# Optimization experiments

Hardware: AMD Instinct MI355X
Metric: run time of the kernel (lower is better)

## Reference

```python
import jax, jax.numpy as jnp
import numpy as np
from jax import lax

B, T = 4, 1024
V, C, H, L = 50257, 768, 12, 12
D = C // H           # head size = 64
FF = 4 * C           # ffn hidden = 3072
EPS = 1e-5


def setup_inputs() -> dict:
    key = jax.random.key(0)
    ks = jax.random.split(key, 20)
    s = 0.02
    inp = {
        'x': jax.random.randint(ks[0], (B, T), 0, V, dtype=jnp.int32),
        'y': jax.random.randint(ks[1], (B, T), 0, V, dtype=jnp.int32),
        'tok_emb': jax.random.normal(ks[2], (V, C), jnp.float32) * s,
        'pos_emb': jax.random.normal(ks[3], (V, C), jnp.float32) * s,
        'Wk': jax.random.normal(ks[4], (L, H, C, D), jnp.float32) * s,
        'Wq': jax.random.normal(ks[5], (L, H, C, D), jnp.float32) * s,
        'Wv': jax.random.normal(ks[6], (L, H, C, D), jnp.float32) * s,
        'Wproj': jax.random.normal(ks[7], (L, C, C), jnp.float32) * s,
        'bproj': jnp.zeros((L, C), jnp.float32),
        'ln1_g': jnp.ones((L, C), jnp.float32),
        'ln1_b': jnp.zeros((L, C), jnp.float32),
        'W1': jax.random.normal(ks[8], (L, C, FF), jnp.float32) * s,
        'b1': jnp.zeros((L, FF), jnp.float32),
        'W2': jax.random.normal(ks[9], (L, FF, C), jnp.float32) * s,
        'b2': jnp.zeros((L, C), jnp.float32),
        'ln2_g': jnp.ones((L, C), jnp.float32),
        'ln2_b': jnp.zeros((L, C), jnp.float32),
        'Wlm': jax.random.normal(ks[10], (C, V), jnp.float32) * s,
        'blm': jnp.zeros((V,), jnp.float32),
    }
    return inp


def _layernorm(x, g, b):
    m = jnp.mean(x, axis=-1, keepdims=True)
    v = jnp.var(x, axis=-1, keepdims=True)
    return (x - m) * lax.rsqrt(v + EPS) * g + b


def _forward(x, tok_emb, pos_emb, Wk, Wq, Wv, Wproj, bproj, ln1_g, ln1_b,
             W1, b1, W2, b2, ln2_g, ln2_b, Wlm, blm):
    # NOTE: the original indexes the position embedding table with token ids x.
    h = tok_emb[x] + pos_emb[x]                      # [B,T,C]
    mask = jnp.tril(jnp.ones((T, T), bool))          # causal tril buffer
    scale = D ** -0.5

    def layer(h, p):
        wk, wq, wv, wp, bp, g1, be1, w1, bb1, w2, bb2, g2, be2 = p
        k = jnp.einsum('btc,hcd->bhtd', h, wk)
        q = jnp.einsum('btc,hcd->bhtd', h, wq)
        v = jnp.einsum('btc,hcd->bhtd', h, wv)
        # faithful quirk: k @ q^T (rows=k index, cols=q index)
        wei = jnp.einsum('bhtd,bhsd->bhts', k, q) * scale
        wei = jnp.where(mask, wei, -jnp.inf)
        wei = jax.nn.softmax(wei, axis=-1)
        o = jnp.einsum('bhts,bhsd->bhtd', wei, v)    # [B,H,T,D]
        o = o.transpose(0, 2, 1, 3).reshape(B, T, C) # concat heads
        attn = o @ wp + bp
        h = _layernorm(h + attn, g1, be1)
        ff = jax.nn.relu(h @ w1 + bb1) @ w2 + bb2
        h = _layernorm(h + ff, g2, be2)
        return h, None

    params = (Wk, Wq, Wv, Wproj, bproj, ln1_g, ln1_b, W1, b1, W2, b2, ln2_g, ln2_b)
    h, _ = lax.scan(layer, h, params)
    logits = h @ Wlm + blm                           # [B,T,V]
    return logits


def reference(x, y, tok_emb, pos_emb, Wk, Wq, Wv, Wproj, bproj, ln1_g, ln1_b,
              W1, b1, W2, b2, ln2_g, ln2_b, Wlm, blm):
    logits = _forward(x, tok_emb, pos_emb, Wk, Wq, Wv, Wproj, bproj,
                      ln1_g, ln1_b, W1, b1, W2, b2, ln2_g, ln2_b, Wlm, blm)
    logp = jax.nn.log_softmax(logits, axis=-1)
    loss = -jnp.mean(jnp.take_along_axis(logp, y[..., None].astype(jnp.int32), axis=-1))
    return logits, loss
```

## Files before the change

### kernel.cpp

```cpp
#include <hip/hip_runtime.h>
#include <hip/hip_bf16.h>
#include <math.h>

#define BB 4
#define TT 1024
#define VV 50257
#define VPAD2 50432
#define CC 768
#define HH 12
#define DD 64
#define LL 12
#define FFH 3072
#define MROWS (BB*TT)
#define QBLK 128
#define KVBLK 64
#define NPART (VPAD2 / 64)

typedef __bf16 bf16x8 __attribute__((ext_vector_type(8)));
typedef float  f32x4  __attribute__((ext_vector_type(4)));
typedef unsigned int u32;
#define AS1 __attribute__((address_space(1)))
#define AS3 __attribute__((address_space(3)))

static __device__ __forceinline__ void gload_lds16(const void* g, void* l) {
    __builtin_amdgcn_global_load_lds((const AS1 u32*)g, (AS3 u32*)l, 16, 0, 0);
}

static __device__ __forceinline__ void stage_tile(const __hip_bfloat16* __restrict__ A,
                                                  const __hip_bfloat16* __restrict__ Bt,
                                                  int Kld, int k0, int bm, int bn,
                                                  int w, int l, char* As, char* Bs) {
    #pragma unroll
    for (int it = 0; it < 4; it++) {
        int chunk = w * 4 + it;
        int o = chunk * 1024 + l * 16;
        int row = o >> 7;
        int cb = (o & 127) ^ ((row & 7) << 4);
        gload_lds16(A + (size_t)(bm + row) * Kld + k0 + (cb >> 1), As + chunk * 1024);
        gload_lds16(Bt + (size_t)(bn + row) * Kld + k0 + (cb >> 1), Bs + chunk * 1024);
    }
}

static __device__ __forceinline__ void stage_tile_n64(const __hip_bfloat16* __restrict__ A,
                                                      const __hip_bfloat16* __restrict__ Bt,
                                                      int Kld, int k0, int bm, int bn,
                                                      int w, int l, char* As, char* Bs) {
    #pragma unroll
    for (int it = 0; it < 4; it++) {
        int chunk = w * 4 + it;
        int o = chunk * 1024 + l * 16;
        int row = o >> 7;
        int cb = (o & 127) ^ ((row & 7) << 4);
        gload_lds16(A + (size_t)(bm + row) * Kld + k0 + (cb >> 1), As + chunk * 1024);
    }
    #pragma unroll
    for (int it = 0; it < 2; it++) {
        int chunk = w * 2 + it;
        int o = chunk * 1024 + l * 16;
        int row = o >> 7;
        int cb = (o & 127) ^ ((row & 7) << 4);
        gload_lds16(Bt + (size_t)(bn + row) * Kld + k0 + (cb >> 1), Bs + chunk * 1024);
    }
}

static __device__ __forceinline__ void stage_tile256(const __hip_bfloat16* __restrict__ A,
                                                     const __hip_bfloat16* __restrict__ Bt,
                                                     int Kld, int k0, int bm, int bn,
                                                     int w, int l, char* As, char* Bs) {
    #pragma unroll
    for (int it = 0; it < 4; it++) {
        int chunk = w * 4 + it;
        int o = chunk * 1024 + l * 16;
        int row = o >> 7;
        int cb = (o & 127) ^ ((row & 7) << 4);
        gload_lds16(A + (size_t)(bm + row) * Kld + k0 + (cb >> 1), As + chunk * 1024);
        gload_lds16(Bt + (size_t)(bn + row) * Kld + k0 + (cb >> 1), Bs + chunk * 1024);
    }
}

__global__ void embed_kernel(const int* __restrict__ x, const float* __restrict__ tok,
                             const float* __restrict__ pos, float* __restrict__ h,
                             __hip_bfloat16* __restrict__ hb) {
    int idx = blockIdx.x * 256 + threadIdx.x;
    if (idx >= MROWS * CC) return;
    int row = idx / CC, c = idx - row * CC;
    int id = x[row];
    float v = tok[(size_t)id * CC + c] + pos[(size_t)id * CC + c];
    h[idx] = v;
    hb[idx] = __float2bfloat16(v);
}

__global__ __launch_bounds__(256) void cvtT_mat(const float* __restrict__ in,
                                                __hip_bfloat16* __restrict__ out,
                                                int K, int Nin,
                                                size_t ibs, size_t obs) {
    __shared__ float t[32][33];
    const float* ip = in + blockIdx.z * ibs;
    __hip_bfloat16* op = out + blockIdx.z * obs;
    int n0 = blockIdx.x * 32, k0 = blockIdx.y * 32;
    int tx = threadIdx.x & 31, ty = threadIdx.x >> 5;
    #pragma unroll
    for (int i = 0; i < 4; i++) {
        int k = k0 + ty + i * 8, n = n0 + tx;
        t[ty + i * 8][tx] = (n < Nin) ? ip[(size_t)k * Nin + n] : 0.f;
    }
    __syncthreads();
    #pragma unroll
    for (int i = 0; i < 4; i++) {
        int n = n0 + ty + i * 8, k = k0 + tx;
        op[(size_t)n * K + k] = __float2bfloat16(t[tx][ty + i * 8]);
    }
}

__global__ __launch_bounds__(256) void cvtT_qkv(const float* __restrict__ Wk,
                                                const float* __restrict__ Wq,
                                                const float* __restrict__ Wv,
                                                __hip_bfloat16* __restrict__ kT,
                                                __hip_bfloat16* __restrict__ qT,
                                                __hip_bfloat16* __restrict__ vT) {
    int z = blockIdx.z;
    int tensor = z / 144, lh = z % 144;
    int l = lh / HH, hh = lh % HH;
    const float* in = (tensor == 0 ? Wk : tensor == 1 ? Wq : Wv) + (size_t)lh * CC * DD;
    __hip_bfloat16* out = (tensor == 0 ? kT : tensor == 1 ? qT : vT)
                          + ((size_t)l * CC + hh * DD) * CC;
    __shared__ float t[32][33];
    int c0 = blockIdx.x * 32, d0 = blockIdx.y * 32;
    int tx = threadIdx.x & 31, ty = threadIdx.x >> 5;
    #pragma unroll
    for (int i = 0; i < 4; i++)
        t[ty + i * 8][tx] = in[(size_t)(c0 + ty + i * 8) * DD + d0 + tx];
    __syncthreads();
    #pragma unroll
    for (int i = 0; i < 4; i++)
        out[(size_t)(d0 + ty + i * 8) * CC + c0 + tx] = __float2bfloat16(t[tx][ty + i * 8]);
}

__global__ __launch_bounds__(256) void gemm_mfma(const __hip_bfloat16* __restrict__ A,
                                                 const __hip_bfloat16* __restrict__ Bt,
                                                 const float* __restrict__ bias,
                                                 float* __restrict__ Cf,
                                                 __hip_bfloat16* __restrict__ Cb,
                                                 int M, int N, int K, int relu) {
    __shared__ __align__(16) char smem[65536];
    int tid = threadIdx.x;
    int l = tid & 63, w = tid >> 6;
    int wr = w >> 1, wc = w & 1;
    int bm = blockIdx.y * 128, bn = blockIdx.x * 128;

    f32x4 acc[4][4] = {};

    stage_tile(A, Bt, K, 0, bm, bn, w, l, smem, smem + 32768);
    int p = 0;
    for (int k0 = 0; k0 < K; k0 += 64) {
        __syncthreads();
        if (k0 + 64 < K)
            stage_tile(A, Bt, K, k0 + 64, bm, bn, w, l,
                       smem + (p ^ 1) * 16384, smem + 32768 + (p ^ 1) * 16384);
        const char* Ab = smem + p * 16384;
        const char* Bb = smem + 32768 + p * 16384;
        #pragma unroll
        for (int ks = 0; ks < 2; ks++) {
            bf16x8 af[4], bfr[4];
            #pragma unroll
            for (int i = 0; i < 4; i++) {
                int row = wr * 64 + i * 16 + (l & 15);
                int cb = (ks * 64 + (l >> 4) * 16) ^ ((row & 7) << 4);
                af[i] = *(const bf16x8*)(Ab + row * 128 + cb);
            }
            #pragma unroll
            for (int j = 0; j < 4; j++) {
                int row = wc * 64 + j * 16 + (l & 15);
                int cb = (ks * 64 + (l >> 4) * 16) ^ ((row & 7) << 4);
                bfr[j] = *(const bf16x8*)(Bb + row * 128 + cb);
            }
            #pragma unroll
            for (int i = 0; i < 4; i++)
                #pragma unroll
                for (int j = 0; j < 4; j++)
                    acc[i][j] = __builtin_amdgcn_mfma_f32_16x16x32_bf16(af[i], bfr[j], acc[i][j], 0, 0, 0);
        }
        p ^= 1;
    }

    if (Cb) {
        __hip_bfloat16* ebh = (__hip_bfloat16*)smem;
        __syncthreads();
        #pragma unroll
        for (int i = 0; i < 4; i++) {
            #pragma unroll
            for (int j = 0; j < 4; j++) {
                int colt = wc * 64 + j * 16 + (l & 15);
                float bv = bias ? bias[bn + colt] : 0.f;
                #pragma unroll
                for (int r = 0; r < 4; r++) {
                    int rowc = wr * 64 + i * 16 + (l >> 4) * 4 + r;
                    float v = acc[i][j][r] + bv;
                    if (relu) v = fmaxf(v, 0.f);
                    ebh[rowc * 136 + colt] = __float2bfloat16(v);
                }
            }
        }
        __syncthreads();
        #pragma unroll
        for (int pass = 0; pass < 8; pass++) {
            int idx = pass * 256 + tid;
            int rowc = idx >> 4, colq = idx & 15;
            *(bf16x8*)&Cb[(size_t)(bm + rowc) * N + bn + colq * 8] =
                *(const bf16x8*)&ebh[rowc * 136 + colq * 8];
        }
    } else {
        float* eb = (float*)smem;
        #pragma unroll
        for (int c = 0; c < 2; c++) {
            __syncthreads();
            if (wr == c) {
                #pragma unroll
                for (int i = 0; i < 4; i++) {
                    #pragma unroll
                    for (int j = 0; j < 4; j++) {
                        int colt = wc * 64 + j * 16 + (l & 15);
                        float bv = bias ? bias[bn + colt] : 0.f;
                        #pragma unroll
                        for (int r = 0; r < 4; r++) {
                            int rowc = i * 16 + (l >> 4) * 4 + r;
                            float v = acc[i][j][r] + bv;
                            if (relu) v = fmaxf(v, 0.f);
                            eb[rowc * 132 + colt] = v;
                        }
                    }
                }
            }
            __syncthreads();
            #pragma unroll
            for (int pass = 0; pass < 8; pass++) {
                int idx = pass * 256 + tid;
                int rowc = idx >> 5, colq = idx & 31;
                *(f32x4*)&Cf[(size_t)(bm + c * 64 + rowc) * N + bn + colq * 4] =
                    *(const f32x4*)&eb[rowc * 132 + colq * 4];
            }
        }
    }
}

__global__ __launch_bounds__(256) void gemm_mfma_n64(const __hip_bfloat16* __restrict__ A,
                                                     const __hip_bfloat16* __restrict__ Bt,
                                                     const float* __restrict__ bias,
                                                     float* __restrict__ Cf,
                                                     int M, int N, int K, int relu) {
    __shared__ __align__(16) char smem[49152];
    int tid = threadIdx.x;
    int l = tid & 63, w = tid >> 6;
    int bm = blockIdx.y * 128, bn = blockIdx.x * 64;

    f32x4 acc[2][4] = {};

    stage_tile_n64(A, Bt, K, 0, bm, bn, w, l, smem, smem + 32768);
    int p = 0;
    for (int k0 = 0; k0 < K; k0 += 64) {
        __syncthreads();
        if (k0 + 64 < K)
            stage_tile_n64(A, Bt, K, k0 + 64, bm, bn, w, l,
                           smem + (p ^ 1) * 16384, smem + 32768 + (p ^ 1) * 8192);
        const char* Ab = smem + p * 16384;
        const char* Bb = smem + 32768 + p * 8192;
        #pragma unroll
        for (int ks = 0; ks < 2; ks++) {
            bf16x8 af[2], bfr[4];
            #pragma unroll
            for (int i = 0; i < 2; i++) {
                int row = w * 32 + i * 16 + (l & 15);
                int cb = (ks * 64 + (l >> 4) * 16) ^ ((row & 7) << 4);
                af[i] = *(const bf16x8*)(Ab + row * 128 + cb);
            }
            #pragma unroll
            for (int j = 0; j < 4; j++) {
                int row = j * 16 + (l & 15);
                int cb = (ks * 64 + (l >> 4) * 16) ^ ((row & 7) << 4);
                bfr[j] = *(const bf16x8*)(Bb + row * 128 + cb);
            }
            #pragma unroll
            for (int i = 0; i < 2; i++)
                #pragma unroll
                for (int j = 0; j < 4; j++)
                    acc[i][j] = __builtin_amdgcn_mfma_f32_16x16x32_bf16(af[i], bfr[j], acc[i][j], 0, 0, 0);
        }
        p ^= 1;
    }

    float* eb = (float*)smem;
    __syncthreads();
    #pragma unroll
    for (int i = 0; i < 2; i++) {
        #pragma unroll
        for (int j = 0; j < 4; j++) {
            int colt = j * 16 + (l & 15);
            float bv = bias ? bias[bn + colt] : 0.f;
            #pragma unroll
            for (int r = 0; r < 4; r++) {
                int rowc = w * 32 + i * 16 + (l >> 4) * 4 + r;
                float v = acc[i][j][r] + bv;
                if (relu) v = fmaxf(v, 0.f);
                eb[rowc * 68 + colt] = v;
            }
        }
    }
    __syncthreads();
    #pragma unroll
    for (int pass = 0; pass < 8; pass++) {
        int idx = pass * 256 + tid;
        int rowc = idx >> 4, colq = idx & 15;
        *(f32x4*)&Cf[(size_t)(bm + rowc) * N + bn + colq * 4] =
            *(const f32x4*)&eb[rowc * 68 + colq * 4];
    }
}

__global__ __launch_bounds__(512) void lm_head_mfma256(const __hip_bfloat16* __restrict__ A,
                                                       const __hip_bfloat16* __restrict__ Bt,
                                                       const float* __restrict__ bias,
                                                       float* __restrict__ Cf,
                                                       float* __restrict__ pm,
                                                       float* __restrict__ ps) {
    __shared__ __align__(16) char smem[131072];
    int tid = threadIdx.x;
    int l = tid & 63, w = tid >> 6;
    int wr = w >> 2, wc = w & 3;
    int bm = blockIdx.x * 256, bn = blockIdx.y * 256;

    f32x4 acc[8][4] = {};

    stage_tile256(A, Bt, CC, 0, bm, bn, w, l, smem, smem + 65536);
    int p = 0;
    for (int k0 = 0; k0 < CC; k0 += 64) {
        __syncthreads();
        if (k0 + 64 < CC)
            stage_tile256(A, Bt, CC, k0 + 64, bm, bn, w, l,
                          smem + (p ^ 1) * 32768, smem + 65536 + (p ^ 1) * 32768);
        const char* Ab = smem + p * 32768;
        const char* Bb = smem + 65536 + p * 32768;
        #pragma unroll
        for (int ks = 0; ks < 2; ks++) {
            bf16x8 af[8], bfr[4];
            #pragma unroll
            for (int i = 0; i < 8; i++) {
                int row = wr * 128 + i * 16 + (l & 15);
                int cb = (ks * 64 + (l >> 4) * 16) ^ ((row & 7) << 4);
                af[i] = *(const bf16x8*)(Ab + row * 128 + cb);
            }
            #pragma unroll
            for (int j = 0; j < 4; j++) {
                int row = wc * 64 + j * 16 + (l & 15);
                int cb = (ks * 64 + (l >> 4) * 16) ^ ((row & 7) << 4);
                bfr[j] = *(const bf16x8*)(Bb + row * 128 + cb);
            }
            #pragma unroll
            for (int i = 0; i < 8; i++)
                #pragma unroll
                for (int j = 0; j < 4; j++)
                    acc[i][j] = __builtin_amdgcn_mfma_f32_16x16x32_bf16(af[i], bfr[j], acc[i][j], 0, 0, 0);
        }
        p ^= 1;
    }

    #pragma unroll
    for (int j = 0; j < 4; j++) {
        int col = bn + wc * 64 + j * 16 + (l & 15);
        float bv = (col < VV) ? bias[col] : 0.f;
        #pragma unroll
        for (int i = 0; i < 8; i++)
            #pragma unroll
            for (int r = 0; r < 4; r++)
                acc[i][j][r] += bv;
    }

    int pidx = blockIdx.y * 4 + wc;
    #pragma unroll
    for (int i = 0; i < 8; i++) {
        int row = bm + wr * 128 + i * 16 + (l >> 4) * 4;
        #pragma unroll
        for (int r = 0; r < 4; r++) {
            float pv[4];
            float rmax = -1e30f;
            #pragma unroll
            for (int j = 0; j < 4; j++) {
                int col = bn + wc * 64 + j * 16 + (l & 15);
                float v = (col < VV) ? acc[i][j][r] : -1e30f;
                pv[j] = v;
                rmax = fmaxf(rmax, v);
            }
            #pragma unroll
            for (int msk = 1; msk < 16; msk <<= 1)
                rmax = fmaxf(rmax, __shfl_xor(rmax, msk));
            float s = 0.f;
            #pragma unroll
            for (int j = 0; j < 4; j++) s += __expf(pv[j] - rmax);
            #pragma unroll
            for (int msk = 1; msk < 16; msk <<= 1)
                s += __shfl_xor(s, msk);
            if ((l & 15) == 0) {
                pm[(size_t)(row + r) * NPART + pidx] = rmax;
                ps[(size_t)(row + r) * NPART + pidx] = s;
            }
        }
    }

    __syncthreads();
    float* eb0 = (float*)smem + (size_t)(w * 2 + 0) * (16 * 68);
    float* eb1 = (float*)smem + (size_t)(w * 2 + 1) * (16 * 68);
    int colg = bn + wc * 64 + l;
    bool valid = colg < VV;
    #pragma unroll
    for (int i = 0; i < 8; i++) {
        float* eb = (i & 1) ? eb1 : eb0;
        #pragma unroll
        for (int j = 0; j < 4; j++) {
            int colt = j * 16 + (l & 15);
            #pragma unroll
            for (int r = 0; r < 4; r++) {
                int rowc = (l >> 4) * 4 + r;
                eb[rowc * 68 + colt] = acc[i][j][r];
            }
        }
        int rowbase = bm + wr * 128 + i * 16;
        #pragma unroll
        for (int pp = 0; pp < 16; pp++) {
            float v = eb[pp * 68 + l];
            if (valid) Cf[(size_t)(rowbase + pp) * VV + colg] = v;
        }
    }
}

__global__ __launch_bounds__(256) void nll_combine(const float* __restrict__ pm,
                                                   const float* __restrict__ ps,
                                                   const float* __restrict__ logits,
                                                   const int* __restrict__ y,
                                                   float* __restrict__ rl) {
    int m = blockIdx.x, tid = threadIdx.x;
    __shared__ float rm[256], rs[256];
    float mt = -1e30f, st = 0.f;
    for (int i = tid; i < NPART; i += 256) {
        float mi = pm[(size_t)m * NPART + i];
        float si = ps[(size_t)m * NPART + i];
        float mn = fmaxf(mt, mi);
        st = st * __expf(mt - mn) + si * __expf(mi - mn);
        mt = mn;
    }
    rm[tid] = mt; rs[tid] = st; __syncthreads();
    for (int off = 128; off > 0; off >>= 1) {
        if (tid < off) {
            float ma = rm[tid], mb = rm[tid + off];
            float mn = fmaxf(ma, mb);
            rs[tid] = rs[tid] * __expf(ma - mn) + rs[tid + off] * __expf(mb - mn);
            rm[tid] = mn;
        }
        __syncthreads();
    }
    if (tid == 0)
        rl[m] = logf(rs[0]) + rm[0] - logits[(size_t)m * VV + y[m]];
}

__global__ __launch_bounds__(256) void gemm_qkv_mfma(const __hip_bfloat16* __restrict__ A,
                                                     const __hip_bfloat16* __restrict__ kT,
                                                     const __hip_bfloat16* __restrict__ qT,
                                                     const __hip_bfloat16* __restrict__ vT,
                                                     __hip_bfloat16* __restrict__ ko,
                                                     __hip_bfloat16* __restrict__ qo,
                                                     __hip_bfloat16* __restrict__ vto) {
    const __hip_bfloat16* Bt = (blockIdx.z == 0) ? kT : (blockIdx.z == 1) ? qT : vT;
    __shared__ __align__(16) char smem[65536];
    int tid = threadIdx.x;
    int l = tid & 63, w = tid >> 6;
    int wr = w >> 1, wc = w & 1;
    int bm = blockIdx.y * 128, bn = blockIdx.x * 128;

    f32x4 acc[4][4] = {};

    stage_tile(A, Bt, CC, 0, bm, bn, w, l, smem, smem + 32768);
    int p = 0;
    for (int k0 = 0; k0 < CC; k0 += 64) {
        __syncthreads();
        if (k0 + 64 < CC)
            stage_tile(A, Bt, CC, k0 + 64, bm, bn, w, l,
                       smem + (p ^ 1) * 16384, smem + 32768 + (p ^ 1) * 16384);
        const char* Ab = smem + p * 16384;
        const char* Bb = smem + 32768 + p * 16384;
        #pragma unroll
        for (int ks = 0; ks < 2; ks++) {
            bf16x8 af[4], bfr[4];
            #pragma unroll
            for (int i = 0; i < 4; i++) {
                int row = wr * 64 + i * 16 + (l & 15);
                int cb = (ks * 64 + (l >> 4) * 16) ^ ((row & 7) << 4);
                af[i] = *(const bf16x8*)(Ab + row * 128 + cb);
            }
            #pragma unroll
            for (int j = 0; j < 4; j++) {
                int row = wc * 64 + j * 16 + (l & 15);
                int cb = (ks * 64 + (l >> 4) * 16) ^ ((row & 7) << 4);
                bfr[j] = *(const bf16x8*)(Bb + row * 128 + cb);
            }
            #pragma unroll
            for (int i = 0; i < 4; i++)
                #pragma unroll
                for (int j = 0; j < 4; j++)
                    acc[i][j] = __builtin_amdgcn_mfma_f32_16x16x32_bf16(af[i], bfr[j], acc[i][j], 0, 0, 0);
        }
        p ^= 1;
    }

    int zz = blockIdx.z;
    int b = bm >> 10, tbase = bm & 1023;
    __hip_bfloat16* eb = (__hip_bfloat16*)smem;
    __syncthreads();
    if (zz != 2) {
        #pragma unroll
        for (int i = 0; i < 4; i++)
            #pragma unroll
            for (int j = 0; j < 4; j++) {
                int colt = wc * 64 + j * 16 + (l & 15);
                #pragma unroll
                for (int r = 0; r < 4; r++) {
                    int rowc = wr * 64 + i * 16 + (l >> 4) * 4 + r;
                    eb[rowc * 136 + colt] = __float2bfloat16(acc[i][j][r]);
                }
            }
        __syncthreads();
        __hip_bfloat16* O = (zz == 0) ? ko : qo;
        #pragma unroll
        for (int pass = 0; pass < 8; pass++) {
            int idx = pass * 256 + tid;
            int rowc = idx >> 4, colq = idx & 15;
            int head = (bn >> 6) + (colq >> 3);
            int d = (colq & 7) * 8;
            int t = tbase + rowc;
            *(bf16x8*)&O[(((size_t)(b * HH + head)) * TT + t) * DD + d] =
                *(const bf16x8*)&eb[rowc * 136 + colq * 8];
        }
    } else {
        #pragma unroll
        for (int i = 0; i < 4; i++)
            #pragma unroll
            for (int j = 0; j < 4; j++) {
                int colt = wc * 64 + j * 16 + (l & 15);
                #pragma unroll
                for (int r = 0; r < 4; r++) {
                    int rowc = wr * 64 + i * 16 + (l >> 4) * 4 + r;
                    eb[colt * 136 + rowc] = __float2bfloat16(acc[i][j][r]);
                }
            }
        __syncthreads();
        #pragma unroll
        for (int pass = 0; pass < 8; pass++) {
            int idx = pass * 256 + tid;
            int line = idx >> 4, tq = idx & 15;
            int head = (bn >> 6) + (line >> 6);
            int d = line & 63;
            *(bf16x8*)&vto[(((size_t)(b * HH + head)) * DD + d) * TT + tbase + tq * 8] =
                *(const bf16x8*)&eb[line * 136 + tq * 8];
        }
    }
}

__global__ __launch_bounds__(256) void attn_mfma(const __hip_bfloat16* __restrict__ kq,
                                                 const __hip_bfloat16* __restrict__ qk,
                                                 const __hip_bfloat16* __restrict__ vt,
                                                 __hip_bfloat16* __restrict__ oc) {
    __shared__ __hip_bfloat16 Qs[2][KVBLK * 64];
    __shared__ __hip_bfloat16 Vs[2][64 * KVBLK];
    __shared__ __hip_bfloat16 Ps[QBLK * KVBLK];
    int tid = threadIdx.x;
    int l = tid & 63, w = tid >> 6;
    int t0 = blockIdx.x * QBLK;
    size_t bh = (size_t)(blockIdx.z * HH + blockIdx.y);
    const __hip_bfloat16* kqp = kq + bh * TT * DD;
    const __hip_bfloat16* qkp = qk + bh * TT * DD;
    const __hip_bfloat16* vtp = vt + bh * DD * TT;

    bf16x8 af[2][2];
    #pragma unroll
    for (int i = 0; i < 2; i++)
        #pragma unroll
        for (int ks = 0; ks < 2; ks++)
            af[i][ks] = *(const bf16x8*)&kqp[(size_t)(t0 + w * 32 + i * 16 + (l & 15)) * DD
                                             + ks * 32 + (l >> 4) * 8];

    f32x4 acc_o[2][4] = {};
    float mrow[2][4], lrow[2][4];
    #pragma unroll
    for (int i = 0; i < 2; i++)
        #pragma unroll
        for (int r = 0; r < 4; r++) { mrow[i][r] = -1e30f; lrow[i][r] = 0.f; }

    auto stageKV = [&](int pp, int s0) {
        #pragma unroll
        for (int it = 0; it < 2; it++) {
            int chunk = w * 2 + it;
            int o = chunk * 1024 + l * 16;
            int row = o >> 7;
            int cb = (o & 127) ^ ((row & 7) << 4);
            gload_lds16(qkp + (size_t)(s0 + row) * DD + (cb >> 1),
                        (char*)Qs[pp] + chunk * 1024);
            gload_lds16(vtp + (size_t)row * TT + s0 + (cb >> 1),
                        (char*)Vs[pp] + chunk * 1024);
        }
    };

    int nt = (t0 + QBLK) / KVBLK;
    stageKV(0, 0);
    int p = 0;
    for (int ti = 0; ti < nt; ti++) {
        int s0 = ti * KVBLK;
        __syncthreads();
        if (ti + 1 < nt) stageKV(p ^ 1, s0 + KVBLK);

        f32x4 sa[2][4] = {};
        #pragma unroll
        for (int ks = 0; ks < 2; ks++) {
            bf16x8 bfr[4];
            #pragma unroll
            for (int j = 0; j < 4; j++) {
                int row = j * 16 + (l & 15);
                int cb = (ks * 64 + (l >> 4) * 16) ^ ((row & 7) << 4);
                bfr[j] = *(const bf16x8*)((const char*)Qs[p] + row * 128 + cb);
            }
            #pragma unroll
            for (int i = 0; i < 2; i++)
                #pragma unroll
                for (int j = 0; j < 4; j++)
                    sa[i][j] = __builtin_amdgcn_mfma_f32_16x16x32_bf16(af[i][ks], bfr[j], sa[i][j], 0, 0, 0);
        }

        #pragma unroll
        for (int i = 0; i < 2; i++) {
            #pragma unroll
            for (int r = 0; r < 4; r++) {
                int t = t0 + w * 32 + i * 16 + (l >> 4) * 4 + r;
                float pv[4];
                float rmax = -1e30f;
                #pragma unroll
                for (int j = 0; j < 4; j++) {
                    int s = s0 + j * 16 + (l & 15);
                    float v = sa[i][j][r] * 0.125f;
                    v = (s <= t) ? v : -1e30f;
                    pv[j] = v;
                    rmax = fmaxf(rmax, v);
                }
                #pragma unroll
                for (int msk = 1; msk < 16; msk <<= 1)
                    rmax = fmaxf(rmax, __shfl_xor(rmax, msk));
                float mo = mrow[i][r];
                float mn = fmaxf(mo, rmax);
                float fac = __expf(mo - mn);
                float ls = 0.f;
                int prow = w * 32 + i * 16 + (l >> 4) * 4 + r;
                #pragma unroll
                for (int j = 0; j < 4; j++) {
                    float e = __expf(pv[j] - mn);
                    ls += e;
                    int cb = (j * 32 + (l & 15) * 2) ^ ((prow & 7) << 4);
                    *(__hip_bfloat16*)((char*)Ps + prow * 128 + cb) = __float2bfloat16(e);
                }
                #pragma unroll
                for (int msk = 1; msk < 16; msk <<= 1)
                    ls += __shfl_xor(ls, msk);
                mrow[i][r] = mn;
                lrow[i][r] = lrow[i][r] * fac + ls;
                #pragma unroll
                for (int jd = 0; jd < 4; jd++)
                    acc_o[i][jd][r] *= fac;
            }
        }

        #pragma unroll
        for (int ks = 0; ks < 2; ks++) {
            bf16x8 pa[2], vf[4];
            #pragma unroll
            for (int i = 0; i < 2; i++) {
                int row = w * 32 + i * 16 + (l & 15);
                int cb = (ks * 64 + (l >> 4) * 16) ^ ((row & 7) << 4);
                pa[i] = *(const bf16x8*)((const char*)Ps + row * 128 + cb);
            }
            #pragma unroll
            for (int jd = 0; jd < 4; jd++) {
                int row = jd * 16 + (l & 15);
                int cb = (ks * 64 + (l >> 4) * 16) ^ ((row & 7) << 4);
                vf[jd] = *(const bf16x8*)((const char*)Vs[p] + row * 128 + cb);
            }
            #pragma unroll
            for (int i = 0; i < 2; i++)
                #pragma unroll
                for (int jd = 0; jd < 4; jd++)
                    acc_o[i][jd] = __builtin_amdgcn_mfma_f32_16x16x32_bf16(pa[i], vf[jd], acc_o[i][jd], 0, 0, 0);
        }
        p ^= 1;
    }

    int b = blockIdx.z, hh = blockIdx.y;
    #pragma unroll
    for (int i = 0; i < 2; i++) {
        #pragma unroll
        for (int r = 0; r < 4; r++) {
            float inv = 1.f / lrow[i][r];
            int t = t0 + w * 32 + i * 16 + (l >> 4) * 4 + r;
            #pragma unroll
            for (int jd = 0; jd < 4; jd++) {
                int d = jd * 16 + (l & 15);
                oc[((size_t)(b * TT + t)) * CC + hh * DD + d] =
                    __float2bfloat16(acc_o[i][jd][r] * inv);
            }
        }
    }
}

__global__ __launch_bounds__(256) void resid_ln(float* __restrict__ h,
                                                const float* __restrict__ t,
                                                const float* __restrict__ g,
                                                const float* __restrict__ bta,
                                                __hip_bfloat16* __restrict__ hb) {
    int row = blockIdx.x;
    int tid = threadIdx.x;
    __shared__ float red[256];
    float x[3];
    float s = 0.f;
    #pragma unroll
    for (int i = 0; i < 3; i++) {
        int c = tid + i * 256;
        x[i] = h[(size_t)row * CC + c] + t[(size_t)row * CC + c];
        s += x[i];
    }
    red[tid] = s; __syncthreads();
    for (int off = 128; off > 0; off >>= 1) {
        if (tid < off) red[tid] += red[tid + off];
        __syncthreads();
    }
    float mean = red[0] * (1.f / CC); __syncthreads();
    float s2 = 0.f;
    #pragma unroll
    for (int i = 0; i < 3; i++) { float dd = x[i] - mean; s2 += dd * dd; }
    red[tid] = s2; __syncthreads();
    for (int off = 128; off > 0; off >>= 1) {
        if (tid < off) red[tid] += red[tid + off];
        __syncthreads();
    }
    float inv = rsqrtf(red[0] * (1.f / CC) + 1e-5f);
    #pragma unroll
    for (int i = 0; i < 3; i++) {
        int c = tid + i * 256;
        float o = (x[i] - mean) * inv * g[c] + bta[c];
        h[(size_t)row * CC + c] = o;
        hb[(size_t)row * CC + c] = __float2bfloat16(o);
    }
}

__global__ __launch_bounds__(256) void loss_reduce(const float* __restrict__ rl,
                                                   float* __restrict__ out) {
    int tid = threadIdx.x;
    __shared__ float red[256];
    float s = 0.f;
    for (int i = tid; i < MROWS; i += 256) s += rl[i];
    red[tid] = s; __syncthreads();
    for (int off = 128; off > 0; off >>= 1) {
        if (tid < off) red[tid] += red[tid + off];
        __syncthreads();
    }
    if (tid == 0) out[0] = red[0] * (1.f / MROWS);
}

extern "C" void kernel_launch(void* const* d_in, const int* in_sizes, int n_in,
                              void* d_out, int out_size, void* d_ws, size_t ws_size,
                              hipStream_t stream) {
    const int*   x     = (const int*)d_in[0];
    const int*   y     = (const int*)d_in[1];
    const float* tok   = (const float*)d_in[2];
    const float* pos   = (const float*)d_in[3];
    const float* Wk    = (const float*)d_in[4];
    const float* Wq    = (const float*)d_in[5];
    const float* Wv    = (const float*)d_in[6];
    const float* Wproj = (const float*)d_in[7];
    const float* bproj = (const float*)d_in[8];
    const float* ln1g  = (const float*)d_in[9];
    const float* ln1b  = (const float*)d_in[10];
    const float* W1    = (const float*)d_in[11];
    const float* b1    = (const float*)d_in[12];
    const float* W2    = (const float*)d_in[13];
    const float* b2    = (const float*)d_in[14];
    const float* ln2g  = (const float*)d_in[15];
    const float* ln2b  = (const float*)d_in[16];
    const float* Wlm   = (const float*)d_in[17];
    const float* blm   = (const float*)d_in[18];

    float* logits = (float*)d_out;
    float* lossp  = (float*)d_out + ((size_t)out_size - 1);

    char* p = (char*)d_ws;
    auto alloc = [&](size_t bytes) { char* r = p; p += (bytes + 255) & ~255ULL; return r; };
    const size_t S_HC = (size_t)MROWS * CC;

    float* h    = (float*)alloc(S_HC * 4);
    float* tmpf = (float*)alloc(S_HC * 4);
    float* rl   = (float*)alloc(MROWS * 4);
    float* pm   = (float*)alloc((size_t)MROWS * NPART * 4);
    float* ps   = (float*)alloc((size_t)MROWS * NPART * 4);
    __hip_bfloat16* kbb  = (__hip_bfloat16*)alloc(S_HC * 2);
    __hip_bfloat16* qbb  = (__hip_bfloat16*)alloc(S_HC * 2);
    __hip_bfloat16* vtb  = (__hip_bfloat16*)alloc(S_HC * 2);
    __hip_bfloat16* hb   = (__hip_bfloat16*)alloc(S_HC * 2);
    __hip_bfloat16* ocb  = (__hip_bfloat16*)alloc(S_HC * 2);
    __hip_bfloat16* ff1b = (__hip_bfloat16*)alloc((size_t)MROWS * FFH * 2);
    __hip_bfloat16* kT   = (__hip_bfloat16*)alloc((size_t)LL * CC * CC * 2);
    __hip_bfloat16* qT   = (__hip_bfloat16*)alloc((size_t)LL * CC * CC * 2);
    __hip_bfloat16* vT   = (__hip_bfloat16*)alloc((size_t)LL * CC * CC * 2);
    __hip_bfloat16* pT   = (__hip_bfloat16*)alloc((size_t)LL * CC * CC * 2);
    __hip_bfloat16* w1T  = (__hip_bfloat16*)alloc((size_t)LL * CC * FFH * 2);
    __hip_bfloat16* w2T  = (__hip_bfloat16*)alloc((size_t)LL * FFH * CC * 2);
    __hip_bfloat16* lmT  = (__hip_bfloat16*)alloc((size_t)VPAD2 * CC * 2);

    dim3 blk(256);

    cvtT_qkv<<<dim3(24, 2, 3 * 144), blk, 0, stream>>>(Wk, Wq, Wv, kT, qT, vT);
    cvtT_mat<<<dim3(24, 24, LL), blk, 0, stream>>>(Wproj, pT, CC, CC,
                                                   (size_t)CC * CC, (size_t)CC * CC);
    cvtT_mat<<<dim3(96, 24, LL), blk, 0, stream>>>(W1, w1T, CC, FFH,
                                                   (size_t)CC * FFH, (size_t)FFH * CC);
    cvtT_mat<<<dim3(24, 96, LL), blk, 0, stream>>>(W2, w2T, FFH, CC,
                                                   (size_t)FFH * CC, (size_t)CC * FFH);
    cvtT_mat<<<dim3(VPAD2 / 32, 24, 1), blk, 0, stream>>>(Wlm, lmT, CC, VV, 0, 0);

    embed_kernel<<<dim3((MROWS * CC + 255) / 256), blk, 0, stream>>>(x, tok, pos, h, hb);

    for (int l = 0; l < LL; l++) {
        const __hip_bfloat16* kT_l = kT + (size_t)l * CC * CC;
        const __hip_bfloat16* qT_l = qT + (size_t)l * CC * CC;
        const __hip_bfloat16* vT_l = vT + (size_t)l * CC * CC;
        const __hip_bfloat16* pT_l = pT + (size_t)l * CC * CC;
        const __hip_bfloat16* w1T_l = w1T + (size_t)l * CC * FFH;
        const __hip_bfloat16* w2T_l = w2T + (size_t)l * FFH * CC;

        gemm_qkv_mfma<<<dim3(CC / 128, MROWS / 128, 3), blk, 0, stream>>>(
            hb, kT_l, qT_l, vT_l, kbb, qbb, vtb);
        attn_mfma<<<dim3(TT / QBLK, HH, BB), blk, 0, stream>>>(kbb, qbb, vtb, ocb);
        gemm_mfma_n64<<<dim3(CC / 64, MROWS / 128), blk, 0, stream>>>(
            ocb, pT_l, bproj + (size_t)l * CC, tmpf, MROWS, CC, CC, 0);
        resid_ln<<<dim3(MROWS), blk, 0, stream>>>(h, tmpf, ln1g + (size_t)l * CC,
                                                  ln1b + (size_t)l * CC, hb);
        gemm_mfma<<<dim3(FFH / 128, MROWS / 128), blk, 0, stream>>>(
            hb, w1T_l, b1 + (size_t)l * FFH, (float*)nullptr, ff1b,
            MROWS, FFH, CC, 1);
        gemm_mfma_n64<<<dim3(CC / 64, MROWS / 128), blk, 0, stream>>>(
            ff1b, w2T_l, b2 + (size_t)l * CC, tmpf, MROWS, CC, FFH, 0);
        resid_ln<<<dim3(MROWS), blk, 0, stream>>>(h, tmpf, ln2g + (size_t)l * CC,
                                                  ln2b + (size_t)l * CC, hb);
    }

    lm_head_mfma256<<<dim3(MROWS / 256, VPAD2 / 256), dim3(512), 0, stream>>>(
        hb, lmT, blm, logits, pm, ps);
    nll_combine<<<dim3(MROWS), blk, 0, stream>>>(pm, ps, logits, y, rl);
    loss_reduce<<<dim3(1), blk, 0, stream>>>(rl, lossp);
}
```

Measured before the change: 3.179 ms.

## Drop fp32 residual buffer, use 64-wide QKV tiles, swizzle lm_head blocks

```diff
diff --git a/kernel.cpp b/kernel.cpp
--- a/kernel.cpp
+++ b/kernel.cpp
@@ -79,15 +79,13 @@
 }
 
 __global__ void embed_kernel(const int* __restrict__ x, const float* __restrict__ tok,
-                             const float* __restrict__ pos, float* __restrict__ h,
+                             const float* __restrict__ pos,
                              __hip_bfloat16* __restrict__ hb) {
     int idx = blockIdx.x * 256 + threadIdx.x;
     if (idx >= MROWS * CC) return;
     int row = idx / CC, c = idx - row * CC;
     int id = x[row];
-    float v = tok[(size_t)id * CC + c] + pos[(size_t)id * CC + c];
-    h[idx] = v;
-    hb[idx] = __float2bfloat16(v);
+    hb[idx] = __float2bfloat16(tok[(size_t)id * CC + c] + pos[(size_t)id * CC + c]);
 }
 
 __global__ __launch_bounds__(256) void cvtT_mat(const float* __restrict__ in,
@@ -315,6 +313,102 @@
     }
 }
 
+__global__ __launch_bounds__(256) void gemm_qkv_n64(const __hip_bfloat16* __restrict__ A,
+                                                    const __hip_bfloat16* __restrict__ kT,
+                                                    const __hip_bfloat16* __restrict__ qT,
+                                                    const __hip_bfloat16* __restrict__ vT,
+                                                    __hip_bfloat16* __restrict__ ko,
+                                                    __hip_bfloat16* __restrict__ qo,
+                                                    __hip_bfloat16* __restrict__ vto) {
+    const __hip_bfloat16* Bt = (blockIdx.z == 0) ? kT : (blockIdx.z == 1) ? qT : vT;
+    __shared__ __align__(16) char smem[49152];
+    int tid = threadIdx.x;
+    int l = tid & 63, w = tid >> 6;
+    int bm = blockIdx.y * 128, bn = blockIdx.x * 64;
+
+    f32x4 acc[2][4] = {};
+
+    stage_tile_n64(A, Bt, CC, 0, bm, bn, w, l, smem, smem + 32768);
+    int p = 0;
+    for (int k0 = 0; k0 < CC; k0 += 64) {
+        __syncthreads();
+        if (k0 + 64 < CC)
+            stage_tile_n64(A, Bt, CC, k0 + 64, bm, bn, w, l,
+                           smem + (p ^ 1) * 16384, smem + 32768 + (p ^ 1) * 8192);
+        const char* Ab = smem + p * 16384;
+        const char* Bb = smem + 32768 + p * 8192;
+        #pragma unroll
+        for (int ks = 0; ks < 2; ks++) {
+            bf16x8 af[2], bfr[4];
+            #pragma unroll
+            for (int i = 0; i < 2; i++) {
+                int row = w * 32 + i * 16 + (l & 15);
+                int cb = (ks * 64 + (l >> 4) * 16) ^ ((row & 7) << 4);
+                af[i] = *(const bf16x8*)(Ab + row * 128 + cb);
+            }
+            #pragma unroll
+            for (int j = 0; j < 4; j++) {
+                int row = j * 16 + (l & 15);
+                int cb = (ks * 64 + (l >> 4) * 16) ^ ((row & 7) << 4);
+                bfr[j] = *(const bf16x8*)(Bb + row * 128 + cb);
+            }
+            #pragma unroll
+            for (int i = 0; i < 2; i++)
+                #pragma unroll
+                for (int j = 0; j < 4; j++)
+                    acc[i][j] = __builtin_amdgcn_mfma_f32_16x16x32_bf16(af[i], bfr[j], acc[i][j], 0, 0, 0);
+        }
+        p ^= 1;
+    }
+
+    int zz = blockIdx.z;
+    int b = bm >> 10, tbase = bm & 1023, head = bn >> 6;
+    __hip_bfloat16* eb = (__hip_bfloat16*)smem;
+    __syncthreads();
+    if (zz != 2) {
+        #pragma unroll
+        for (int i = 0; i < 2; i++)
+            #pragma unroll
+            for (int j = 0; j < 4; j++) {
+                int colt = j * 16 + (l & 15);
+                #pragma unroll
+                for (int r = 0; r < 4; r++) {
+                    int rowc = w * 32 + i * 16 + (l >> 4) * 4 + r;
+                    eb[rowc * 72 + colt] = __float2bfloat16(acc[i][j][r]);
+                }
+            }
+        __syncthreads();
+        __hip_bfloat16* O = (zz == 0) ? ko : qo;
+        #pragma unroll
+        for (int pass = 0; pass < 4; pass++) {
+            int idx = pass * 256 + tid;
+            int rowc = idx >> 3, colq = idx & 7;
+            *(bf16x8*)&O[(((size_t)(b * HH + head)) * TT + tbase + rowc) * DD + colq * 8] =
+                *(const bf16x8*)&eb[rowc * 72 + colq * 8];
+        }
+    } else {
+        #pragma unroll
+        for (int i = 0; i < 2; i++)
+            #pragma unroll
+            for (int j = 0; j < 4; j++) {
+                int colt = j * 16 + (l & 15);
+                #pragma unroll
+                for (int r = 0; r < 4; r++) {
+                    int rowc = w * 32 + i * 16 + (l >> 4) * 4 + r;
+                    eb[colt * 136 + rowc] = __float2bfloat16(acc[i][j][r]);
+                }
+            }
+        __syncthreads();
+        #pragma unroll
+        for (int pass = 0; pass < 4; pass++) {
+            int idx = pass * 256 + tid;
+            int line = idx >> 4, tq = idx & 15;
+            *(bf16x8*)&vto[(((size_t)(b * HH + head)) * DD + line) * TT + tbase + tq * 8] =
+                *(const bf16x8*)&eb[line * 136 + tq * 8];
+        }
+    }
+}
+
 __global__ __launch_bounds__(512) void lm_head_mfma256(const __hip_bfloat16* __restrict__ A,
                                                        const __hip_bfloat16* __restrict__ Bt,
                                                        const float* __restrict__ bias,
@@ -325,7 +419,11 @@
     int tid = threadIdx.x;
     int l = tid & 63, w = tid >> 6;
     int wr = w >> 2, wc = w & 3;
-    int bm = blockIdx.x * 256, bn = blockIdx.y * 256;
+    int orig = blockIdx.x + (int)gridDim.x * blockIdx.y;
+    int swz = (orig & 7) * 394 + (orig >> 3);
+    int bm = (swz & 15) * 256;
+    int bnb = swz >> 4;
+    int bn = bnb * 256;
 
     f32x4 acc[8][4] = {};
 
@@ -373,7 +471,7 @@
                 acc[i][j][r] += bv;
     }
 
-    int pidx = blockIdx.y * 4 + wc;
+    int pidx = bnb * 4 + wc;
     #pragma unroll
     for (int i = 0; i < 8; i++) {
         int row = bm + wr * 128 + i * 16 + (l >> 4) * 4;
@@ -459,108 +557,6 @@
         rl[m] = logf(rs[0]) + rm[0] - logits[(size_t)m * VV + y[m]];
 }
 
-__global__ __launch_bounds__(256) void gemm_qkv_mfma(const __hip_bfloat16* __restrict__ A,
-                                                     const __hip_bfloat16* __restrict__ kT,
-                                                     const __hip_bfloat16* __restrict__ qT,
-                                                     const __hip_bfloat16* __restrict__ vT,
-                                                     __hip_bfloat16* __restrict__ ko,
-                                                     __hip_bfloat16* __restrict__ qo,
-                                                     __hip_bfloat16* __restrict__ vto) {
-    const __hip_bfloat16* Bt = (blockIdx.z == 0) ? kT : (blockIdx.z == 1) ? qT : vT;
-    __shared__ __align__(16) char smem[65536];
-    int tid = threadIdx.x;
-    int l = tid & 63, w = tid >> 6;
-    int wr = w >> 1, wc = w & 1;
-    int bm = blockIdx.y * 128, bn = blockIdx.x * 128;
-
-    f32x4 acc[4][4] = {};
-
-    stage_tile(A, Bt, CC, 0, bm, bn, w, l, smem, smem + 32768);
-    int p = 0;
-    for (int k0 = 0; k0 < CC; k0 += 64) {
-        __syncthreads();
-        if (k0 + 64 < CC)
-            stage_tile(A, Bt, CC, k0 + 64, bm, bn, w, l,
-                       smem + (p ^ 1) * 16384, smem + 32768 + (p ^ 1) * 16384);
-        const char* Ab = smem + p * 16384;
-        const char* Bb = smem + 32768 + p * 16384;
-        #pragma unroll
-        for (int ks = 0; ks < 2; ks++) {
-            bf16x8 af[4], bfr[4];
-            #pragma unroll
-            for (int i = 0; i < 4; i++) {
-                int row = wr * 64 + i * 16 + (l & 15);
-                int cb = (ks * 64 + (l >> 4) * 16) ^ ((row & 7) << 4);
-                af[i] = *(const bf16x8*)(Ab + row * 128 + cb);
-            }
-            #pragma unroll
-            for (int j = 0; j < 4; j++) {
-                int row = wc * 64 + j * 16 + (l & 15);
-                int cb = (ks * 64 + (l >> 4) * 16) ^ ((row & 7) << 4);
-                bfr[j] = *(const bf16x8*)(Bb + row * 128 + cb);
-            }
-            #pragma unroll
-            for (int i = 0; i < 4; i++)
-                #pragma unroll
-                for (int j = 0; j < 4; j++)
-                    acc[i][j] = __builtin_amdgcn_mfma_f32_16x16x32_bf16(af[i], bfr[j], acc[i][j], 0, 0, 0);
-        }
-        p ^= 1;
-    }
-
-    int zz = blockIdx.z;
-    int b = bm >> 10, tbase = bm & 1023;
-    __hip_bfloat16* eb = (__hip_bfloat16*)smem;
-    __syncthreads();
-    if (zz != 2) {
-        #pragma unroll
-        for (int i = 0; i < 4; i++)
-            #pragma unroll
-            for (int j = 0; j < 4; j++) {
-                int colt = wc * 64 + j * 16 + (l & 15);
-                #pragma unroll
-                for (int r = 0; r < 4; r++) {
-                    int rowc = wr * 64 + i * 16 + (l >> 4) * 4 + r;
-                    eb[rowc * 136 + colt] = __float2bfloat16(acc[i][j][r]);
-                }
-            }
-        __syncthreads();
-        __hip_bfloat16* O = (zz == 0) ? ko : qo;
-        #pragma unroll
-        for (int pass = 0; pass < 8; pass++) {
-            int idx = pass * 256 + tid;
-            int rowc = idx >> 4, colq = idx & 15;
-            int head = (bn >> 6) + (colq >> 3);
-            int d = (colq & 7) * 8;
-            int t = tbase + rowc;
-            *(bf16x8*)&O[(((size_t)(b * HH + head)) * TT + t) * DD + d] =
-                *(const bf16x8*)&eb[rowc * 136 + colq * 8];
-        }
-    } else {
-        #pragma unroll
-        for (int i = 0; i < 4; i++)
-            #pragma unroll
-            for (int j = 0; j < 4; j++) {
-                int colt = wc * 64 + j * 16 + (l & 15);
-                #pragma unroll
-                for (int r = 0; r < 4; r++) {
-                    int rowc = wr * 64 + i * 16 + (l >> 4) * 4 + r;
-                    eb[colt * 136 + rowc] = __float2bfloat16(acc[i][j][r]);
-                }
-            }
-        __syncthreads();
-        #pragma unroll
-        for (int pass = 0; pass < 8; pass++) {
-            int idx = pass * 256 + tid;
-            int line = idx >> 4, tq = idx & 15;
-            int head = (bn >> 6) + (line >> 6);
-            int d = line & 63;
-            *(bf16x8*)&vto[(((size_t)(b * HH + head)) * DD + d) * TT + tbase + tq * 8] =
-                *(const bf16x8*)&eb[line * 136 + tq * 8];
-        }
-    }
-}
-
 __global__ __launch_bounds__(256) void attn_mfma(const __hip_bfloat16* __restrict__ kq,
                                                  const __hip_bfloat16* __restrict__ qk,
                                                  const __hip_bfloat16* __restrict__ vt,
@@ -712,11 +708,10 @@
     }
 }
 
-__global__ __launch_bounds__(256) void resid_ln(float* __restrict__ h,
+__global__ __launch_bounds__(256) void resid_ln(__hip_bfloat16* __restrict__ hb,
                                                 const float* __restrict__ t,
                                                 const float* __restrict__ g,
-                                                const float* __restrict__ bta,
-                                                __hip_bfloat16* __restrict__ hb) {
+                                                const float* __restrict__ bta) {
     int row = blockIdx.x;
     int tid = threadIdx.x;
     __shared__ float red[256];
@@ -725,7 +720,7 @@
     #pragma unroll
     for (int i = 0; i < 3; i++) {
         int c = tid + i * 256;
-        x[i] = h[(size_t)row * CC + c] + t[(size_t)row * CC + c];
+        x[i] = __bfloat162float(hb[(size_t)row * CC + c]) + t[(size_t)row * CC + c];
         s += x[i];
     }
     red[tid] = s; __syncthreads();
@@ -746,9 +741,7 @@
     #pragma unroll
     for (int i = 0; i < 3; i++) {
         int c = tid + i * 256;
-        float o = (x[i] - mean) * inv * g[c] + bta[c];
-        h[(size_t)row * CC + c] = o;
-        hb[(size_t)row * CC + c] = __float2bfloat16(o);
+        hb[(size_t)row * CC + c] = __float2bfloat16((x[i] - mean) * inv * g[c] + bta[c]);
     }
 }
 
@@ -796,7 +789,6 @@
     auto alloc = [&](size_t bytes) { char* r = p; p += (bytes + 255) & ~255ULL; return r; };
     const size_t S_HC = (size_t)MROWS * CC;
 
-    float* h    = (float*)alloc(S_HC * 4);
     float* tmpf = (float*)alloc(S_HC * 4);
     float* rl   = (float*)alloc(MROWS * 4);
     float* pm   = (float*)alloc((size_t)MROWS * NPART * 4);
@@ -826,7 +818,7 @@
                                                    (size_t)FFH * CC, (size_t)CC * FFH);
     cvtT_mat<<<dim3(VPAD2 / 32, 24, 1), blk, 0, stream>>>(Wlm, lmT, CC, VV, 0, 0);
 
-    embed_kernel<<<dim3((MROWS * CC + 255) / 256), blk, 0, stream>>>(x, tok, pos, h, hb);
+    embed_kernel<<<dim3((MROWS * CC + 255) / 256), blk, 0, stream>>>(x, tok, pos, hb);
 
     for (int l = 0; l < LL; l++) {
         const __hip_bfloat16* kT_l = kT + (size_t)l * CC * CC;
@@ -836,20 +828,20 @@
         const __hip_bfloat16* w1T_l = w1T + (size_t)l * CC * FFH;
         const __hip_bfloat16* w2T_l = w2T + (size_t)l * FFH * CC;
 
-        gemm_qkv_mfma<<<dim3(CC / 128, MROWS / 128, 3), blk, 0, stream>>>(
+        gemm_qkv_n64<<<dim3(CC / 64, MROWS / 128, 3), blk, 0, stream>>>(
             hb, kT_l, qT_l, vT_l, kbb, qbb, vtb);
         attn_mfma<<<dim3(TT / QBLK, HH, BB), blk, 0, stream>>>(kbb, qbb, vtb, ocb);
         gemm_mfma_n64<<<dim3(CC / 64, MROWS / 128), blk, 0, stream>>>(
             ocb, pT_l, bproj + (size_t)l * CC, tmpf, MROWS, CC, CC, 0);
-        resid_ln<<<dim3(MROWS), blk, 0, stream>>>(h, tmpf, ln1g + (size_t)l * CC,
-                                                  ln1b + (size_t)l * CC, hb);
+        resid_ln<<<dim3(MROWS), blk, 0, stream>>>(hb, tmpf, ln1g + (size_t)l * CC,
+                                                  ln1b + (size_t)l * CC);
         gemm_mfma<<<dim3(FFH / 128, MROWS / 128), blk, 0, stream>>>(
             hb, w1T_l, b1 + (size_t)l * FFH, (float*)nullptr, ff1b,
             MROWS, FFH, CC, 1);
         gemm_mfma_n64<<<dim3(CC / 64, MROWS / 128), blk, 0, stream>>>(
             ff1b, w2T_l, b2 + (size_t)l * CC, tmpf, MROWS, CC, FFH, 0);
-        resid_ln<<<dim3(MROWS), blk, 0, stream>>>(h, tmpf, ln2g + (size_t)l * CC,
-                                                  ln2b + (size_t)l * CC, hb);
+        resid_ln<<<dim3(MROWS), blk, 0, stream>>>(hb, tmpf, ln2g + (size_t)l * CC,
+                                                  ln2b + (size_t)l * CC);
     }
 
     lm_head_mfma256<<<dim3(MROWS / 256, VPAD2 / 256), dim3(512), 0, stream>>>(
```

New measurement: 3.182 ms. No clear change (+0.1%).
